# Kernel tuning notes

Hardware: AMD Instinct MI355X
Metric: run time of the kernel (lower is better)

Reference implementation:

```python
import jax, jax.numpy as jnp
import numpy as np

N, E, F, H, C1, C2, G, NC = 50000, 800000, 512, 2, 128, 128, 8, 4
D1, D2 = H * C1, H * C2  # 256, 256


def setup_inputs() -> dict:
    key = jax.random.key(0)
    ks = jax.random.split(key, 32)
    w = lambda k, shape: jax.random.normal(k, shape, jnp.float32) * 0.02
    inp = {
        'x': jax.random.normal(ks[0], (N, F), jnp.float32),
        'edge_index': jax.random.randint(ks[1], (2, E), 0, N),
        'batch': jnp.sort(jax.random.randint(ks[2], (N,), 0, G)),
        # TransformerConv layer 1: in=F, heads=H, out_per_head=C1 (concat)
        'wq1': w(ks[3], (F, D1)), 'bq1': w(ks[4], (D1,)),
        'wk1': w(ks[5], (F, D1)), 'bk1': w(ks[6], (D1,)),
        'wv1': w(ks[7], (F, D1)), 'bv1': w(ks[8], (D1,)),
        'ws1': w(ks[9], (F, D1)), 'bs1': w(ks[10], (D1,)),
        # TransformerConv layer 2: in=D1, heads=H, out_per_head=C2 (concat)
        'wq2': w(ks[11], (D1, D2)), 'bq2': w(ks[12], (D2,)),
        'wk2': w(ks[13], (D1, D2)), 'bk2': w(ks[14], (D2,)),
        'wv2': w(ks[15], (D1, D2)), 'bv2': w(ks[16], (D2,)),
        'ws2': w(ks[17], (D1, D2)), 'bs2': w(ks[18], (D2,)),
        # fc head: Linear(D2 -> C2//2), Linear(C2//2 -> NC)
        'wf1': w(ks[19], (D2, C2 // 2)), 'bf1': w(ks[20], (C2 // 2,)),
        'wf2': w(ks[21], (C2 // 2, NC)), 'bf2': w(ks[22], (NC,)),
    }
    return inp


def transformer_conv(x, src, dst, wq, bq, wk, bk, wv, bv, ws, bs, heads, ch):
    """PyG TransformerConv (concat=True, root_weight=True, beta=False)."""
    n = x.shape[0]
    q = (x @ wq + bq).reshape(n, heads, ch)
    k = (x @ wk + bk).reshape(n, heads, ch)
    v = (x @ wv + bv).reshape(n, heads, ch)
    scale = 1.0 / np.sqrt(ch).astype(np.float32)
    # per-edge attention score: [E, H]
    score = jnp.einsum('ehc,ehc->eh', q[dst], k[src]) * scale
    # segment softmax over incoming edges of each target node
    m = jax.lax.stop_gradient(jax.ops.segment_max(score, dst, num_segments=n))
    ex = jnp.exp(score - m[dst])
    denom = jax.ops.segment_sum(ex, dst, num_segments=n)
    alpha = ex / (denom[dst] + 1e-16)  # [E, H]
    agg = jax.ops.segment_sum(alpha[:, :, None] * v[src], dst, num_segments=n)
    return agg.reshape(n, heads * ch) + (x @ ws + bs)


def reference(x, edge_index, batch,
              wq1, bq1, wk1, bk1, wv1, bv1, ws1, bs1,
              wq2, bq2, wk2, bk2, wv2, bv2, ws2, bs2,
              wf1, bf1, wf2, bf2):
    src, dst = edge_index[0], edge_index[1]
    h = jax.nn.relu(transformer_conv(x, src, dst, wq1, bq1, wk1, bk1, wv1, bv1, ws1, bs1, H, C1))
    h = jax.nn.relu(transformer_conv(h, src, dst, wq2, bq2, wk2, bk2, wv2, bv2, ws2, bs2, H, C2))
    pooled = jax.ops.segment_max(h, batch, num_segments=G)  # global_max_pool -> [G, D2]
    return (pooled @ wf1 + bf1) @ wf2 + bf2  # [G, NC]
```

## Files before the change

### kernel.cpp

```cpp
#include <hip/hip_runtime.h>
#include <cstdio>

#define Nn 50000
#define Ee 800000
#define Ff 512
#define Dd 256
#define Gg 8
#define SCANB 49

typedef short short8 __attribute__((ext_vector_type(8)));
typedef __bf16 bf16x8 __attribute__((ext_vector_type(8)));
typedef float f32x4 __attribute__((ext_vector_type(4)));
typedef _Float16 half2v __attribute__((ext_vector_type(2)));

#if defined(__has_builtin)
#if __has_builtin(__builtin_amdgcn_cvt_f32_fp8)
#define HAS_CVTFP8 1
#endif
#endif

__device__ inline unsigned short f2bf(float f) {
  unsigned u = __float_as_uint(f);
  u += 0x7FFFu + ((u >> 16) & 1u);
  return (unsigned short)(u >> 16);
}
__device__ inline float bf2f(unsigned short h) {
  return __uint_as_float(((unsigned)h) << 16);
}

__device__ inline unsigned char f2fp8(float f) {
  const float af = fabsf(f);
  const unsigned s = (f < 0.f) ? 0x80u : 0u;
  if (af >= 448.f) return (unsigned char)(s | 0x7E);
  if (af < 0.015625f) {
    int q = (int)(af * 512.f + 0.5f);
    return (unsigned char)(s | q);
  }
  unsigned u = __float_as_uint(af);
  unsigned m = u & 0x7fffffu;
  unsigned e = u >> 23;
  unsigned r = m + 0x7ffffu + ((m >> 20) & 1u);
  if (r >> 23) { e += 1; r = 0; }
  unsigned em = ((e - 120u) << 3) | ((r >> 20) & 7u);
  if (em > 0x7Eu) em = 0x7Eu;
  return (unsigned char)(s | em);
}

template <int SEL>
__device__ inline float fp8tof(unsigned v) {
#ifdef HAS_CVTFP8
  return __builtin_amdgcn_cvt_f32_fp8(v, SEL);
#else
  unsigned b = (v >> (SEL * 8)) & 0xffu;
  unsigned em = b & 0x7fu;
  float n = __uint_as_float((em << 20) + 0x3C000000u);
  float dn = (float)em * 0.001953125f;
  float r = (em < 8u) ? dn : n;
  return (b & 0x80u) ? -r : r;
#endif
}

__device__ inline void gload16(const void* g, void* l) {
  __builtin_amdgcn_global_load_lds((const __attribute__((address_space(1))) void*)g,
                                   (__attribute__((address_space(3))) void*)l, 16, 0, 0);
}


__global__ void hist_kernel(const int* __restrict__ dst, int* __restrict__ deg,
                            int* __restrict__ rank) {
  int i = blockIdx.x * blockDim.x + threadIdx.x;
  int stride = gridDim.x * blockDim.x;
  for (; i < Ee; i += stride) rank[i] = atomicAdd(&deg[dst[i]], 1);
}

__global__ __launch_bounds__(1024) void scan1_kernel(const int* __restrict__ deg,
                                                     int* __restrict__ off,
                                                     int* __restrict__ bsum) {
  __shared__ int wsum[16];
  int tid = threadIdx.x, lane = tid & 63, w = tid >> 6;
  int i = blockIdx.x * 1024 + tid;
  int v = (i < Nn) ? deg[i] : 0;
  int x = v;
#pragma unroll
  for (int o = 1; o < 64; o <<= 1) {
    int t = __shfl_up(x, o);
    if (lane >= o) x += t;
  }
  if (lane == 63) wsum[w] = x;
  __syncthreads();
  if (w == 0 && lane < 16) {
    int y = wsum[lane];
#pragma unroll
    for (int o = 1; o < 16; o <<= 1) {
      int t = __shfl_up(y, o);
      if (lane >= o) y += t;
    }
    wsum[lane] = y;
  }
  __syncthreads();
  int incl = x + (w ? wsum[w - 1] : 0);
  if (i < Nn) off[i] = incl - v;
  if (tid == 1023) bsum[blockIdx.x] = incl;
}

__global__ void scan2_kernel(const int* __restrict__ bsum, int* __restrict__ boff,
                             int* __restrict__ offN) {
  int lane = threadIdx.x;
  int v = (lane < SCANB) ? bsum[lane] : 0;
  int x = v;
#pragma unroll
  for (int o = 1; o < 64; o <<= 1) {
    int t = __shfl_up(x, o);
    if (lane >= o) x += t;
  }
  if (lane < SCANB) boff[lane] = x - v;
  if (lane == 63) *offN = x;
}

__global__ void scan3_kernel(int* __restrict__ off, const int* __restrict__ boff) {
  int i = blockIdx.x * 256 + threadIdx.x;
  if (i < Nn) off[i] += boff[i >> 10];
}

__global__ void scatter_kernel(const int* __restrict__ src, const int* __restrict__ dst,
                               const int* __restrict__ off, const int* __restrict__ rank,
                               int* __restrict__ ssrc) {
  int i = blockIdx.x * blockDim.x + threadIdx.x;
  int stride = gridDim.x * blockDim.x;
  for (; i < Ee; i += stride) {
    ssrc[off[dst[i]] + rank[i]] = src[i];
  }
}


__global__ void round_kernel(const float* __restrict__ in, unsigned short* __restrict__ out,
                             int M, int K) {
  const int kg4 = K >> 2;
  int i = blockIdx.x * blockDim.x + threadIdx.x;
  const int total = M * kg4;
  const int stride = gridDim.x * blockDim.x;
  for (; i < total; i += stride) {
    const int row = i / kg4, kg = i - row * kg4;
    const float4 v = *(const float4*)(in + (size_t)row * K + kg * 4);
    ushort4 h;
    h.x = f2bf(v.x); h.y = f2bf(v.y); h.z = f2bf(v.z); h.w = f2bf(v.w);
    *(ushort4*)(out + (size_t)row * K + kg * 4) = h;
  }
}

__global__ void convw_kernel(const float* __restrict__ W0, const float* __restrict__ W1,
                             const float* __restrict__ W2, const float* __restrict__ W3,
                             unsigned short* __restrict__ B, int K) {
  int i = blockIdx.x * blockDim.x + threadIdx.x;
  const int total = 1024 * K;
  const int stride = gridDim.x * blockDim.x;
  for (; i < total; i += stride) {
    const int n = i & 1023;
    const int k = i >> 10;
    const int z = n >> 8, c = n & 255;
    const float* W = z == 0 ? W0 : z == 1 ? W1 : z == 2 ? W2 : W3;
    B[(size_t)n * K + k] = f2bf(W[(size_t)k * Dd + c]);
  }
}


__global__ __launch_bounds__(256, 6)
void gemm_mfma(const unsigned short* __restrict__ A2, int M, int K,
               const unsigned short* __restrict__ B,
               const float* __restrict__ b0, const float* __restrict__ b1,
               const float* __restrict__ b2, const float* __restrict__ b3,
               _Float16* __restrict__ qout, unsigned char* __restrict__ kvout,
               _Float16* __restrict__ sout) {
  __shared__ __align__(16) char smem[32768];
  unsigned short* As = (unsigned short*)smem;
  unsigned short* Bs = (unsigned short*)(smem + 16384);
  const int tid = threadIdx.x;
  const int lane = tid & 63, w = tid >> 6;
  const int wr = w >> 1, wc = w & 1;
  const int p = blockIdx.x;
  const int xcd = p & 7;
  const int i2 = p >> 3;
  const int bm = (xcd * 49 + (i2 >> 3)) * 128;
  const int zblk = (i2 & 7) >> 1;
  const int colbase = (i2 & 1) * 128;
  const int lda = K, ldb = K;
  const int nsteps = K >> 6;
  const int srow = lane >> 3, sslot = lane & 7;
  const int fr = lane & 15, fq = lane >> 4;

  f32x4 acc[4][4] = {};

  for (int s = 0; s < nsteps; ++s) {
    const int kk = s << 6;
    __syncthreads();
#pragma unroll
    for (int h = 0; h < 4; ++h) {
      const int q = h * 4 + w;
      const int r = q * 8 + srow;
      const int g = sslot ^ (r & 7);
      int ga = bm + r; if (ga > M - 1) ga = M - 1;
      gload16(A2 + (size_t)ga * lda + kk + g * 8, (char*)As + q * 1024);
      const int gb = (zblk * 256 + colbase) + r;
      gload16(B + (size_t)gb * ldb + kk + g * 8, (char*)Bs + q * 1024);
    }
    __syncthreads();
    short8 av[2][4], bv[2][4];
#pragma unroll
    for (int kh = 0; kh < 2; ++kh)
#pragma unroll
      for (int i = 0; i < 4; ++i) {
        const int ra = wr * 64 + i * 16 + fr;
        av[kh][i] = *(const short8*)((const char*)As + ra * 128 + (((kh * 4 + fq) ^ (ra & 7)) << 4));
        const int rb = wc * 64 + i * 16 + fr;
        bv[kh][i] = *(const short8*)((const char*)Bs + rb * 128 + (((kh * 4 + fq) ^ (rb & 7)) << 4));
      }
#pragma unroll
    for (int kh = 0; kh < 2; ++kh)
#pragma unroll
      for (int mi = 0; mi < 4; ++mi)
#pragma unroll
        for (int ni = 0; ni < 4; ++ni)
          acc[mi][ni] = __builtin_amdgcn_mfma_f32_16x16x32_bf16(
              __builtin_bit_cast(bf16x8, av[kh][mi]),
              __builtin_bit_cast(bf16x8, bv[kh][ni]), acc[mi][ni], 0, 0, 0);
  }

  const float* bp = zblk == 0 ? b0 : zblk == 1 ? b1 : zblk == 2 ? b2 : b3;
  __syncthreads();
  if (zblk == 1 || zblk == 2) {
    unsigned char* S8 = (unsigned char*)smem;
#pragma unroll
    for (int mi = 0; mi < 4; ++mi)
#pragma unroll
      for (int ni = 0; ni < 4; ++ni) {
        const int col = wc * 64 + ni * 16 + fr;
        const float bias = bp[colbase + col];
#pragma unroll
        for (int j = 0; j < 4; ++j) {
          const int row = wr * 64 + mi * 16 + fq * 4 + j;
          S8[row * 256 + (col ^ ((row & 7) << 4))] = f2fp8(acc[mi][ni][j] + bias);
        }
      }
  } else {
#pragma unroll
    for (int mi = 0; mi < 4; ++mi)
#pragma unroll
      for (int ni = 0; ni < 4; ++ni) {
        const int col = wc * 64 + ni * 16 + fr;
        const float bias = bp[colbase + col];
#pragma unroll
        for (int j = 0; j < 4; ++j) {
          const int row = wr * 64 + mi * 16 + fq * 4 + j;
          *(_Float16*)(smem + row * 256 + ((col * 2) ^ ((row & 7) << 4))) =
              (_Float16)(acc[mi][ni][j] + bias);
        }
      }
  }
  __syncthreads();

  const int row = tid >> 1, half = tid & 1;
  const int grow = bm + row;
  if (grow < M) {
    const int sh = (row & 7) << 4;
    if (zblk == 1 || zblk == 2) {
      uint4* dstp = (uint4*)(kvout + (size_t)grow * 512 + (zblk == 2 ? 256 : 0) +
                             colbase + half * 64);
#pragma unroll
      for (int k = 0; k < 4; ++k)
        dstp[k] = *(const uint4*)(smem + row * 256 + ((half * 64 + k * 16) ^ sh));
    } else {
      char* dbase = zblk == 0 ? (char*)qout + (size_t)grow * 512 + colbase * 2
                              : (char*)sout + (size_t)grow * 512 + colbase * 2;
      uint4* dstp = (uint4*)(dbase + half * 128);
#pragma unroll
      for (int k = 0; k < 8; ++k)
        dstp[k] = *(const uint4*)(smem + row * 256 + ((half * 128 + k * 16) ^ sh));
    }
  }
}


__global__ __launch_bounds__(256)
void attn_kernel(const _Float16* __restrict__ qbuf, const unsigned char* __restrict__ kvb,
                 const _Float16* __restrict__ sbuf, const int* __restrict__ off,
                 const int* __restrict__ ssrc, unsigned short* __restrict__ hbout) {
  int gw = (int)((blockIdx.x * 256 + threadIdx.x) >> 6);
  if (gw >= Nn) return;
  int lane = threadIdx.x & 63;

  const uint2 qv = *(const uint2*)(qbuf + (size_t)gw * Dd + lane * 4);
  const half2v q01 = __builtin_bit_cast(half2v, qv.x);
  const half2v q23 = __builtin_bit_cast(half2v, qv.y);
  const float qx = (float)q01[0], qy = (float)q01[1];
  const float qz = (float)q23[0], qw = (float)q23[1];
  int e0 = off[gw], e1 = off[gw + 1];
  const float scale = 0.08838834764831845f;

  float m = -3.4e38f, d = 0.f;
  float ax = 0.f, ay = 0.f, az = 0.f, aw = 0.f;

  for (int e = e0; e < e1; e += 8) {
    int sx[8];
#pragma unroll
    for (int t = 0; t < 8; ++t) {
      const int ee = e + t;
      sx[t] = ssrc[ee < e1 ? ee : e1 - 1];
    }
    unsigned kw[8], vw[8];
#pragma unroll
    for (int t = 0; t < 8; ++t) {
      const unsigned char* row = kvb + (size_t)sx[t] * 512;
      kw[t] = *(const unsigned*)(row + lane * 4);
      vw[t] = *(const unsigned*)(row + 256 + lane * 4);
    }
    float p[8];
#pragma unroll
    for (int t = 0; t < 8; ++t) {
      float pp = qx * fp8tof<0>(kw[t]);
      pp = fmaf(qy, fp8tof<1>(kw[t]), pp);
      pp = fmaf(qz, fp8tof<2>(kw[t]), pp);
      pp = fmaf(qw, fp8tof<3>(kw[t]), pp);
      p[t] = pp;
    }
#pragma unroll
    for (int o = 16; o >= 1; o >>= 1)
#pragma unroll
      for (int t = 0; t < 8; ++t) p[t] += __shfl_xor(p[t], o);
    float sc[8];
#pragma unroll
    for (int t = 0; t < 8; ++t)
      sc[t] = (e + t < e1) ? p[t] * scale : -3.0e38f;
    float mx = m;
#pragma unroll
    for (int t = 0; t < 8; ++t) mx = fmaxf(mx, sc[t]);
    const float f = __expf(m - mx);
    float wsum = 0.f, vx = 0.f, vy = 0.f, vz = 0.f, vww = 0.f;
#pragma unroll
    for (int t = 0; t < 8; ++t) {
      const float wt = __expf(sc[t] - mx);
      wsum += wt;
      vx = fmaf(wt, fp8tof<0>(vw[t]), vx);
      vy = fmaf(wt, fp8tof<1>(vw[t]), vy);
      vz = fmaf(wt, fp8tof<2>(vw[t]), vz);
      vww = fmaf(wt, fp8tof<3>(vw[t]), vww);
    }
    d = d * f + wsum;
    ax = ax * f + vx;
    ay = ay * f + vy;
    az = az * f + vz;
    aw = aw * f + vww;
    m = mx;
  }

  float inv = 1.f / (d + 1e-16f);
  const uint2 sv = *(const uint2*)(sbuf + (size_t)gw * Dd + lane * 4);
  const half2v s01 = __builtin_bit_cast(half2v, sv.x);
  const half2v s23 = __builtin_bit_cast(half2v, sv.y);
  ushort4 hh;
  hh.x = f2bf(fmaxf(fmaf(ax, inv, (float)s01[0]), 0.f));
  hh.y = f2bf(fmaxf(fmaf(ay, inv, (float)s01[1]), 0.f));
  hh.z = f2bf(fmaxf(fmaf(az, inv, (float)s23[0]), 0.f));
  hh.w = f2bf(fmaxf(fmaf(aw, inv, (float)s23[1]), 0.f));
  *(ushort4*)(hbout + (size_t)gw * Dd + lane * 4) = hh;
}


__global__ __launch_bounds__(256)
void pool_kernel(const unsigned short* __restrict__ h, const int* __restrict__ batch,
                 float* __restrict__ pooled) {
  int c = threadIdx.x;
  int n0 = blockIdx.x * 128;
  int n1 = min(n0 + 128, Nn);
  int curg = batch[n0];
  float mx = 0.f;
  for (int n = n0; n < n1; ++n) {
    int g = batch[n];
    if (g != curg) {
      atomicMax((int*)(pooled + curg * Dd + c), __float_as_int(mx));
      mx = 0.f;
      curg = g;
    }
    mx = fmaxf(mx, bf2f(h[(size_t)n * Dd + c]));
  }
  atomicMax((int*)(pooled + curg * Dd + c), __float_as_int(mx));
}

__global__ __launch_bounds__(512)
void fc_kernel(const float* __restrict__ pooled,
               const float* __restrict__ wf1, const float* __restrict__ bf1,
               const float* __restrict__ wf2, const float* __restrict__ bf2,
               float* __restrict__ outp) {
  __shared__ float t[Gg][64];
  int tid = threadIdx.x;
  int g = tid >> 6, j = tid & 63;
  float acc = bf1[j];
  for (int c = 0; c < Dd; ++c) acc = fmaf(pooled[g * Dd + c], wf1[c * 64 + j], acc);
  t[g][j] = acc;
  __syncthreads();
  if (tid < Gg * 4) {
    int gg = tid >> 2, cc = tid & 3;
    float a2 = bf2[cc];
    for (int j2 = 0; j2 < 64; ++j2) a2 = fmaf(t[gg][j2], wf2[j2 * 4 + cc], a2);
    outp[gg * 4 + cc] = a2;
  }
}


extern "C" void kernel_launch(void* const* d_in, const int* in_sizes, int n_in,
                              void* d_out, int out_size, void* d_ws, size_t ws_size,
                              hipStream_t stream) {
  const float* x   = (const float*)d_in[0];
  const int* ei    = (const int*)d_in[1];
  const int* srcE  = ei;
  const int* dstE  = ei + Ee;
  const int* batch = (const int*)d_in[2];
  const float* wq1 = (const float*)d_in[3];  const float* bq1 = (const float*)d_in[4];
  const float* wk1 = (const float*)d_in[5];  const float* bk1 = (const float*)d_in[6];
  const float* wv1 = (const float*)d_in[7];  const float* bv1 = (const float*)d_in[8];
  const float* ws1 = (const float*)d_in[9];  const float* bs1 = (const float*)d_in[10];
  const float* wq2 = (const float*)d_in[11]; const float* bq2 = (const float*)d_in[12];
  const float* wk2 = (const float*)d_in[13]; const float* bk2 = (const float*)d_in[14];
  const float* wv2 = (const float*)d_in[15]; const float* bv2 = (const float*)d_in[16];
  const float* ws2 = (const float*)d_in[17]; const float* bs2 = (const float*)d_in[18];
  const float* wf1 = (const float*)d_in[19]; const float* bf1 = (const float*)d_in[20];
  const float* wf2 = (const float*)d_in[21]; const float* bf2 = (const float*)d_in[22];
  float* outp = (float*)d_out;
  char* ws = (char*)d_ws;

  auto al256 = [](size_t v) { return (v + 255) & ~(size_t)255; };
  size_t o_deg  = 0;
  size_t o_pool = o_deg + (size_t)Nn * 4;
  size_t zbytes = o_pool + (size_t)Gg * Dd * 4;
  size_t o_off  = al256(zbytes);
  size_t o_ssrc = al256(o_off + (size_t)(Nn + 1) * 4);
  size_t o_rank = al256(o_ssrc + (size_t)Ee * 4);
  size_t o_q    = al256(o_rank + (size_t)Ee * 4);
  size_t o_kv   = al256(o_q + (size_t)Nn * Dd * 2);
  size_t o_s    = al256(o_kv + (size_t)Nn * 512);
  size_t o_b1   = al256(o_s + (size_t)Nn * Dd * 2);
  size_t o_b2   = al256(o_b1 + (size_t)1024 * Ff * 2);
  size_t o_a    = al256(o_b2 + (size_t)1024 * Dd * 2);
  size_t o_bsum = al256(o_a + (size_t)Nn * Ff * 2);
  size_t o_boff = al256(o_bsum + (size_t)SCANB * 4);
  size_t total  = o_boff + (size_t)SCANB * 4;
  if (ws_size < total) {
    fprintf(stderr, "kernel_launch: ws too small: %zu < %zu\n", ws_size, total);
    return;
  }

  int*   deg    = (int*)(ws + o_deg);
  float* pooled = (float*)(ws + o_pool);
  int*   off    = (int*)(ws + o_off);
  int*   ssrc   = (int*)(ws + o_ssrc);
  int*   rank   = (int*)(ws + o_rank);
  _Float16* qb  = (_Float16*)(ws + o_q);
  unsigned char* kvb = (unsigned char*)(ws + o_kv);
  _Float16* sb  = (_Float16*)(ws + o_s);
  unsigned short* b1 = (unsigned short*)(ws + o_b1);
  unsigned short* b2 = (unsigned short*)(ws + o_b2);
  unsigned short* a2  = (unsigned short*)(ws + o_a);
  unsigned short* hb  = (unsigned short*)(ws + o_a);
  int* bsum     = (int*)(ws + o_bsum);
  int* boff     = (int*)(ws + o_boff);

  (void)hipMemsetAsync(ws, 0, zbytes, stream);
  hist_kernel<<<1024, 256, 0, stream>>>(dstE, deg, rank);
  scan1_kernel<<<SCANB, 1024, 0, stream>>>(deg, off, bsum);
  scan2_kernel<<<1, 64, 0, stream>>>(bsum, boff, off + Nn);
  scan3_kernel<<<(Nn + 255) / 256, 256, 0, stream>>>(off, boff);
  scatter_kernel<<<1024, 256, 0, stream>>>(srcE, dstE, off, rank, ssrc);

  convw_kernel<<<1024, 256, 0, stream>>>(wq1, wk1, wv1, ws1, b1, Ff);
  convw_kernel<<<1024, 256, 0, stream>>>(wq2, wk2, wv2, ws2, b2, Dd);
  round_kernel<<<4096, 256, 0, stream>>>(x, a2, Nn, Ff);

  gemm_mfma<<<3136, 256, 0, stream>>>(a2, Nn, Ff, b1, bq1, bk1, bv1, bs1, qb, kvb, sb);
  attn_kernel<<<(Nn + 3) / 4, 256, 0, stream>>>(qb, kvb, sb, off, ssrc, hb);
  gemm_mfma<<<3136, 256, 0, stream>>>(hb, Nn, Dd, b2, bq2, bk2, bv2, bs2, qb, kvb, sb);
  attn_kernel<<<(Nn + 3) / 4, 256, 0, stream>>>(qb, kvb, sb, off, ssrc, hb);

  pool_kernel<<<(Nn + 127) / 128, 256, 0, stream>>>(hb, batch, pooled);
  fc_kernel<<<1, 512, 0, stream>>>(pooled, wf1, bf1, wf2, bf2, outp);
}
```

Measured before the change: 482.2 us.

## Split attention wave into two half-waves processing alternate edges with packed fp8 conversion

The attention kernel now splits each 64-lane wave into two 32-lane halves. Each lane covers 8 channels and each half handles alternating edges of the node, so every gather loads 8 bytes per lane instead of 4. The halves keep separate online-softmax states and merge them with a cross-half shuffle at the end, and fp8 decoding uses the packed two-value convert builtin. This aims to halve the per-edge shuffle reduction depth and instruction overhead and to widen the memory accesses. In exchange it adds a final merge step and more registers per lane.

```diff
diff --git a/kernel.cpp b/kernel.cpp
--- a/kernel.cpp
+++ b/kernel.cpp
@@ -11,11 +11,15 @@
 typedef short short8 __attribute__((ext_vector_type(8)));
 typedef __bf16 bf16x8 __attribute__((ext_vector_type(8)));
 typedef float f32x4 __attribute__((ext_vector_type(4)));
+typedef float f32x2 __attribute__((ext_vector_type(2)));
 typedef _Float16 half2v __attribute__((ext_vector_type(2)));
 
 #if defined(__has_builtin)
 #if __has_builtin(__builtin_amdgcn_cvt_f32_fp8)
 #define HAS_CVTFP8 1
+#endif
+#if __has_builtin(__builtin_amdgcn_cvt_pk_f32_fp8)
+#define HAS_PKFP8 1
 #endif
 #endif
 
@@ -57,6 +61,18 @@
   float dn = (float)em * 0.001953125f;
   float r = (em < 8u) ? dn : n;
   return (b & 0x80u) ? -r : r;
+#endif
+}
+
+template <bool HI>
+__device__ inline f32x2 pk8(unsigned w) {
+#ifdef HAS_PKFP8
+  return __builtin_amdgcn_cvt_pk_f32_fp8((int)w, HI);
+#else
+  f32x2 r;
+  if (HI) { r[0] = fp8tof<2>(w); r[1] = fp8tof<3>(w); }
+  else    { r[0] = fp8tof<0>(w); r[1] = fp8tof<1>(w); }
+  return r;
 #endif
 }
 
@@ -284,84 +300,123 @@
 void attn_kernel(const _Float16* __restrict__ qbuf, const unsigned char* __restrict__ kvb,
                  const _Float16* __restrict__ sbuf, const int* __restrict__ off,
                  const int* __restrict__ ssrc, unsigned short* __restrict__ hbout) {
-  int gw = (int)((blockIdx.x * 256 + threadIdx.x) >> 6);
+  const int gw = (int)((blockIdx.x * 256 + threadIdx.x) >> 6);
   if (gw >= Nn) return;
-  int lane = threadIdx.x & 63;
-
-  const uint2 qv = *(const uint2*)(qbuf + (size_t)gw * Dd + lane * 4);
-  const half2v q01 = __builtin_bit_cast(half2v, qv.x);
-  const half2v q23 = __builtin_bit_cast(half2v, qv.y);
-  const float qx = (float)q01[0], qy = (float)q01[1];
-  const float qz = (float)q23[0], qw = (float)q23[1];
-  int e0 = off[gw], e1 = off[gw + 1];
+  const int lane = threadIdx.x & 63;
+  const int half = lane >> 5;
+  const int hl = lane & 31;
   const float scale = 0.08838834764831845f;
 
+  const uint4 qv = *(const uint4*)((const char*)qbuf + (size_t)gw * 512 + hl * 16);
+  float qf[8];
+  {
+    const half2v h0 = __builtin_bit_cast(half2v, qv.x);
+    const half2v h1 = __builtin_bit_cast(half2v, qv.y);
+    const half2v h2 = __builtin_bit_cast(half2v, qv.z);
+    const half2v h3 = __builtin_bit_cast(half2v, qv.w);
+    qf[0] = h0[0]; qf[1] = h0[1]; qf[2] = h1[0]; qf[3] = h1[1];
+    qf[4] = h2[0]; qf[5] = h2[1]; qf[6] = h3[0]; qf[7] = h3[1];
+  }
+
+  const int e0 = off[gw], e1 = off[gw + 1];
   float m = -3.4e38f, d = 0.f;
-  float ax = 0.f, ay = 0.f, az = 0.f, aw = 0.f;
+  float acc[8] = {};
 
   for (int e = e0; e < e1; e += 8) {
-    int sx[8];
-#pragma unroll
-    for (int t = 0; t < 8; ++t) {
-      const int ee = e + t;
+    int sx[4];
+    float vald[4];
+#pragma unroll
+    for (int t = 0; t < 4; ++t) {
+      const int ee = e + 2 * t + half;
+      vald[t] = (ee < e1) ? 1.f : 0.f;
       sx[t] = ssrc[ee < e1 ? ee : e1 - 1];
     }
-    unsigned kw[8], vw[8];
-#pragma unroll
-    for (int t = 0; t < 8; ++t) {
+    uint2 ku[4], vu[4];
+#pragma unroll
+    for (int t = 0; t < 4; ++t) {
       const unsigned char* row = kvb + (size_t)sx[t] * 512;
-      kw[t] = *(const unsigned*)(row + lane * 4);
-      vw[t] = *(const unsigned*)(row + 256 + lane * 4);
-    }
-    float p[8];
-#pragma unroll
-    for (int t = 0; t < 8; ++t) {
-      float pp = qx * fp8tof<0>(kw[t]);
-      pp = fmaf(qy, fp8tof<1>(kw[t]), pp);
-      pp = fmaf(qz, fp8tof<2>(kw[t]), pp);
-      pp = fmaf(qw, fp8tof<3>(kw[t]), pp);
+      ku[t] = *(const uint2*)(row + hl * 8);
+      vu[t] = *(const uint2*)(row + 256 + hl * 8);
+    }
+    float p[4];
+#pragma unroll
+    for (int t = 0; t < 4; ++t) {
+      const f32x2 k01 = pk8<false>(ku[t].x), k23 = pk8<true>(ku[t].x);
+      const f32x2 k45 = pk8<false>(ku[t].y), k67 = pk8<true>(ku[t].y);
+      float pp = qf[0] * k01[0];
+      pp = fmaf(qf[1], k01[1], pp);
+      pp = fmaf(qf[2], k23[0], pp);
+      pp = fmaf(qf[3], k23[1], pp);
+      pp = fmaf(qf[4], k45[0], pp);
+      pp = fmaf(qf[5], k45[1], pp);
+      pp = fmaf(qf[6], k67[0], pp);
+      pp = fmaf(qf[7], k67[1], pp);
       p[t] = pp;
     }
 #pragma unroll
-    for (int o = 16; o >= 1; o >>= 1)
-#pragma unroll
-      for (int t = 0; t < 8; ++t) p[t] += __shfl_xor(p[t], o);
-    float sc[8];
-#pragma unroll
-    for (int t = 0; t < 8; ++t)
-      sc[t] = (e + t < e1) ? p[t] * scale : -3.0e38f;
+    for (int o = 8; o >= 1; o >>= 1)
+#pragma unroll
+      for (int t = 0; t < 4; ++t) p[t] += __shfl_xor(p[t], o);
+    float sct[4];
+#pragma unroll
+    for (int t = 0; t < 4; ++t)
+      sct[t] = vald[t] ? p[t] * scale : -3.4e38f;
     float mx = m;
 #pragma unroll
-    for (int t = 0; t < 8; ++t) mx = fmaxf(mx, sc[t]);
+    for (int t = 0; t < 4; ++t) mx = fmaxf(mx, sct[t]);
     const float f = __expf(m - mx);
-    float wsum = 0.f, vx = 0.f, vy = 0.f, vz = 0.f, vww = 0.f;
-#pragma unroll
-    for (int t = 0; t < 8; ++t) {
-      const float wt = __expf(sc[t] - mx);
+    float wsum = 0.f;
+    float vacc[8] = {};
+#pragma unroll
+    for (int t = 0; t < 4; ++t) {
+      const float wt = __expf(sct[t] - mx) * vald[t];
       wsum += wt;
-      vx = fmaf(wt, fp8tof<0>(vw[t]), vx);
-      vy = fmaf(wt, fp8tof<1>(vw[t]), vy);
-      vz = fmaf(wt, fp8tof<2>(vw[t]), vz);
-      vww = fmaf(wt, fp8tof<3>(vw[t]), vww);
+      const f32x2 v01 = pk8<false>(vu[t].x), v23 = pk8<true>(vu[t].x);
+      const f32x2 v45 = pk8<false>(vu[t].y), v67 = pk8<true>(vu[t].y);
+      vacc[0] = fmaf(wt, v01[0], vacc[0]);
+      vacc[1] = fmaf(wt, v01[1], vacc[1]);
+      vacc[2] = fmaf(wt, v23[0], vacc[2]);
+      vacc[3] = fmaf(wt, v23[1], vacc[3]);
+      vacc[4] = fmaf(wt, v45[0], vacc[4]);
+      vacc[5] = fmaf(wt, v45[1], vacc[5]);
+      vacc[6] = fmaf(wt, v67[0], vacc[6]);
+      vacc[7] = fmaf(wt, v67[1], vacc[7]);
     }
     d = d * f + wsum;
-    ax = ax * f + vx;
-    ay = ay * f + vy;
-    az = az * f + vz;
-    aw = aw * f + vww;
+#pragma unroll
+    for (int j = 0; j < 8; ++j) acc[j] = fmaf(acc[j], f, vacc[j]);
     m = mx;
   }
 
-  float inv = 1.f / (d + 1e-16f);
-  const uint2 sv = *(const uint2*)(sbuf + (size_t)gw * Dd + lane * 4);
-  const half2v s01 = __builtin_bit_cast(half2v, sv.x);
-  const half2v s23 = __builtin_bit_cast(half2v, sv.y);
-  ushort4 hh;
-  hh.x = f2bf(fmaxf(fmaf(ax, inv, (float)s01[0]), 0.f));
-  hh.y = f2bf(fmaxf(fmaf(ay, inv, (float)s01[1]), 0.f));
-  hh.z = f2bf(fmaxf(fmaf(az, inv, (float)s23[0]), 0.f));
-  hh.w = f2bf(fmaxf(fmaf(aw, inv, (float)s23[1]), 0.f));
-  *(ushort4*)(hbout + (size_t)gw * Dd + lane * 4) = hh;
+  {
+    const float m2 = __shfl_xor(m, 32);
+    const float d2 = __shfl_xor(d, 32);
+    float acc2[8];
+#pragma unroll
+    for (int j = 0; j < 8; ++j) acc2[j] = __shfl_xor(acc[j], 32);
+    const float M = fmaxf(m, m2);
+    const float f1 = __expf(m - M);
+    const float f2 = __expf(m2 - M);
+    d = d * f1 + d2 * f2;
+#pragma unroll
+    for (int j = 0; j < 8; ++j) acc[j] = acc[j] * f1 + acc2[j] * f2;
+  }
+
+  if (half == 0) {
+    const float inv = 1.f / (d + 1e-16f);
+    const uint4 sv = *(const uint4*)((const char*)sbuf + (size_t)gw * 512 + hl * 16);
+    const half2v s0 = __builtin_bit_cast(half2v, sv.x);
+    const half2v s1 = __builtin_bit_cast(half2v, sv.y);
+    const half2v s2 = __builtin_bit_cast(half2v, sv.z);
+    const half2v s3 = __builtin_bit_cast(half2v, sv.w);
+    const float sf[8] = {(float)s0[0], (float)s0[1], (float)s1[0], (float)s1[1],
+                         (float)s2[0], (float)s2[1], (float)s3[0], (float)s3[1]};
+    unsigned short ob[8];
+#pragma unroll
+    for (int j = 0; j < 8; ++j)
+      ob[j] = f2bf(fmaxf(fmaf(acc[j], inv, sf[j]), 0.f));
+    *(uint4*)((char*)hbout + (size_t)gw * 512 + hl * 16) = *(const uint4*)ob;
+  }
 }
 
 
```

New measurement: 453.9 us. -5.9%, faster.
